# Optimization experiments

Measured on AMD Instinct MI355X. Metric: run time of the kernel, lower is better.

The kernel has to match this reference:

```python
import jax, jax.numpy as jnp
import numpy as np

B, N, E = 32, 128, 8192        # graphs, nodes/graph, edges total
IN, ED, H = 64, 32, 128        # node feat, edge feat, hidden
K1, K2, K3 = 64, 32, 16        # ceil(0.5*N) cascade from TopKPooling(ratio=0.5)
EPS = 1e-5


def setup_inputs():
    key = jax.random.key(0)
    ks = jax.random.split(key, 20)
    def rn(i, shape, s=1.0):
        return jax.random.normal(ks[i], shape, dtype=jnp.float32) * s
    x = rn(0, (B * N, IN))
    edge_attr = rn(1, (E, ED))
    epg = E // B  # edges per graph (intra-graph only)
    src = jax.random.randint(ks[2], (B, epg), 0, N)
    dst = jax.random.randint(ks[3], (B, epg), 0, N)
    off = (jnp.arange(B) * N)[:, None]
    edge_index = jnp.stack([(src + off).reshape(-1), (dst + off).reshape(-1)]).astype(jnp.int32)
    batch = jnp.repeat(jnp.arange(B), N).astype(jnp.int32)
    p = {}
    p['nn1_w'] = rn(4, (ED, IN * H), 0.05); p['nn1_b'] = jnp.zeros((IN * H,), jnp.float32)
    p['root1'] = rn(5, (IN, H), 0.1);       p['bias1'] = jnp.zeros((H,), jnp.float32)
    p['nn2_w'] = rn(6, (ED, H * H), 0.05);  p['nn2_b'] = jnp.zeros((H * H,), jnp.float32)
    p['root2'] = rn(7, (H, H), 0.1);        p['bias2'] = jnp.zeros((H,), jnp.float32)
    p['nn3_w'] = rn(8, (ED, H * H), 0.05);  p['nn3_b'] = jnp.zeros((H * H,), jnp.float32)
    p['root3'] = rn(9, (H, H), 0.1);        p['bias3'] = jnp.zeros((H,), jnp.float32)
    for k in ('1', '2', '3'):
        p['gamma' + k] = jnp.ones((H,), jnp.float32)
        p['beta' + k] = jnp.zeros((H,), jnp.float32)
    p['pw1'] = rn(10, (H,), 0.1); p['pw2'] = rn(11, (H,), 0.1); p['pw3'] = rn(12, (H,), 0.1)
    p['lin1_w'] = rn(13, (H, H // 2), 0.1); p['lin1_b'] = jnp.zeros((H // 2,), jnp.float32)
    p['lin2_w'] = rn(14, (H // 2, 1), 0.1); p['lin2_b'] = jnp.zeros((1,), jnp.float32)
    return dict(x=x, edge_index=edge_index, edge_attr=edge_attr, batch=batch, **p)


def _nnconv(x, src, dst, emask, eattr, nn_w, nn_b, root, bias, cin, cout, n_nodes):
    # per-edge weight matrix from edge MLP: [E, cin, cout]
    w = (eattr @ nn_w + nn_b).reshape(-1, cin, cout)
    msg = jnp.einsum('ei,eio->eo', x[src], w) * emask[:, None]  # per-edge matvec
    agg = jnp.zeros((n_nodes, cout), x.dtype).at[dst].add(msg)  # scatter-add aggr
    return agg + x @ root + bias


def _bn(x, gamma, beta):
    mu = x.mean(0)
    var = x.var(0)
    return gamma * (x - mu) * jax.lax.rsqrt(var + EPS) + beta


def _topk_pool(x, src, dst, emask, pw, nb, npg, k):
    # PyG TopKPooling: score = tanh((x.p)/||p||); keep top ceil(ratio*n) per graph
    score = jnp.tanh((x @ pw) / jnp.linalg.norm(pw))            # [nb*npg]
    _, idx = jax.lax.top_k(score.reshape(nb, npg), k)           # [nb, k]
    perm = (idx + (jnp.arange(nb) * npg)[:, None]).reshape(-1)  # global node ids
    x_new = x[perm] * score[perm][:, None]
    mapping = jnp.full((nb * npg,), -1, jnp.int32).at[perm].set(
        jnp.arange(nb * k, dtype=jnp.int32))
    ns, nd = mapping[src], mapping[dst]
    valid = (ns >= 0) & (nd >= 0) & emask   # filter_adj via mask, static shapes
    return x_new, jnp.where(valid, ns, 0), jnp.where(valid, nd, 0), valid


def _forward(x, edge_attr, nn1_w, nn1_b, root1, bias1, gamma1, beta1, pw1,
             nn2_w, nn2_b, root2, bias2, gamma2, beta2, pw2,
             nn3_w, nn3_b, root3, bias3, gamma3, beta3, pw3,
             lin1_w, lin1_b, lin2_w, lin2_b, edge_index):
    src0, dst0 = edge_index[0], edge_index[1]
    m0 = jnp.ones((E,), bool)
    h = _nnconv(x, src0, dst0, m0, edge_attr, nn1_w, nn1_b, root1, bias1, IN, H, B * N)
    h = jax.nn.relu(_bn(h, gamma1, beta1))
    h, s1, d1, m1 = _topk_pool(h, src0, dst0, m0, pw1, B, N, K1)
    h = _nnconv(h, s1, d1, m1, edge_attr, nn2_w, nn2_b, root2, bias2, H, H, B * K1)
    h = jax.nn.relu(_bn(h, gamma2, beta2))
    h, s2, d2, m2 = _topk_pool(h, s1, d1, m1, pw2, B, K1, K2)
    h = _nnconv(h, s2, d2, m2, edge_attr, nn3_w, nn3_b, root3, bias3, H, H, B * K2)
    h = jax.nn.relu(_bn(h, gamma3, beta3))
    h, _, _, _ = _topk_pool(h, s2, d2, m2, pw3, B, K2, K3)
    g = h.reshape(B, K3, H).mean(axis=1)          # global_mean_pool (equal-size graphs)
    g = jax.nn.relu(g @ lin1_w + lin1_b)          # dropout is identity in eval mode
    return jax.nn.sigmoid(g @ lin2_w + lin2_b)    # [B, 1]


def reference(x, edge_index, edge_attr, batch,
              nn1_w, nn1_b, root1, bias1, nn2_w, nn2_b, root2, bias2,
              nn3_w, nn3_b, root3, bias3, gamma1, beta1, gamma2, beta2,
              gamma3, beta3, pw1, pw2, pw3, lin1_w, lin1_b, lin2_w, lin2_b):
    return _forward(x, edge_attr, nn1_w, nn1_b, root1, bias1, gamma1, beta1, pw1,
                    nn2_w, nn2_b, root2, bias2, gamma2, beta2, pw2,
                    nn3_w, nn3_b, root3, bias3, gamma3, beta3, pw3,
                    lin1_w, lin1_b, lin2_w, lin2_b, edge_index)
```

## Files before the change

kernel.cpp:

```cpp
#include <hip/hip_runtime.h>

#define E_TOT 8192
#define NB    32
#define H     128
#define EPG   256
#define NDT   34
#define YD    33
#define YCOLS (YD * H)

#define KH1   2176
#define TROW1 (2 * KH1)
#define KSPLIT1 12

typedef __attribute__((ext_vector_type(8))) short bf16x8;
typedef __attribute__((ext_vector_type(4))) float f32x4;

__device__ __forceinline__ unsigned short bf16_rne(float f) {
    unsigned int u = __float_as_uint(f);
    unsigned int r = (u + 0x7FFFu + ((u >> 16) & 1u)) >> 16;
    return (unsigned short)r;
}
__device__ __forceinline__ float bf16_to_f32(unsigned short h) {
    return __uint_as_float(((unsigned int)h) << 16);
}

__device__ __forceinline__ void gload_lds16(const void* g, void* l) {
    __builtin_amdgcn_global_load_lds(
        (const __attribute__((address_space(1))) unsigned int*)g,
        (__attribute__((address_space(3))) unsigned int*)l, 16, 0, 0);
}

__device__ __forceinline__ void sig_done(int* cnt) {
    __syncthreads();
    if (threadIdx.x == 0) { __threadfence(); atomicAdd(cnt, 1); }
}
__device__ __forceinline__ void wait_done(int* cnt, int target) {
    if (threadIdx.x == 0)
        while (atomicAdd(cnt, 0) < target) __builtin_amdgcn_s_sleep(8);
    __syncthreads();
    __threadfence();
}

union PrepSMem {
    struct { unsigned short HI[128][72]; unsigned short LO[128][72]; } b1;
    struct { unsigned short HI[128][40]; unsigned short LO[128][40]; } bt;
    struct { float xL[128][64]; float eaL[256][32]; short srcL[256];
             short lists[16][256]; int cnt[16]; } t1;
};

__global__ __launch_bounds__(256)
void prep_all(const float* __restrict__ x, const float* __restrict__ ea,
              const int* __restrict__ esrc, const int* __restrict__ edst,
              const float* __restrict__ nn1w, const float* __restrict__ nn1b,
              const float* __restrict__ root1,
              const float* __restrict__ nn2w, const float* __restrict__ nn2b,
              const float* __restrict__ root2,
              const float* __restrict__ nn3w, const float* __restrict__ nn3b,
              const float* __restrict__ root3,
              unsigned short* __restrict__ Bt1, unsigned short* __restrict__ Bt2,
              unsigned short* __restrict__ Bt3, unsigned short* __restrict__ T1,
              float* __restrict__ stats, int* __restrict__ cnts)
{
    __shared__ PrepSMem sm;
    const int b   = blockIdx.x;
    const int tid = threadIdx.x;

    if (b < 34) {
        if (b == 0) {
            for (int i = tid; i < 768; i += 256) stats[i] = 0.f;
            if (tid < 8) cnts[tid] = 0;
        }
        const int d = b;
        const float* __restrict__ W =
            (d < 32) ? (nn1w + (size_t)d * 8192) : ((d == 32) ? nn1b : root1);
        for (int idx = tid; idx < 64 * 128; idx += 256) {
            const int ii = idx >> 7, o = idx & 127;
            const float v = W[ii * 128 + o];
            const unsigned short h = bf16_rne(v);
            sm.b1.HI[o][ii] = h;
            sm.b1.LO[o][ii] = bf16_rne(v - bf16_to_f32(h));
        }
        __syncthreads();
        const int o = tid & 127, half = tid >> 7;
        const uint4* s4 = (const uint4*)(half ? &sm.b1.LO[o][0] : &sm.b1.HI[o][0]);
        uint4* d4 = (uint4*)(Bt1 + (size_t)o * TROW1 + (half ? KH1 : 0) + d * 64);
        #pragma unroll
        for (int q = 0; q < 8; ++q) d4[q] = s4[q];
    } else if (b < 306) {
        const int unit  = b - 34;
        const int stage = unit / 136;
        const int u2    = unit - stage * 136;
        const int d  = u2 >> 2;
        const int i0 = (u2 & 3) * 32;
        const float* __restrict__ W = (stage == 0)
            ? ((d < 32) ? (nn2w + (size_t)d * 16384) : ((d == 32) ? nn2b : root2))
            : ((d < 32) ? (nn3w + (size_t)d * 16384) : ((d == 32) ? nn3b : root3));
        unsigned short* __restrict__ Bt = (stage == 0) ? Bt2 : Bt3;

        for (int idx = tid; idx < 32 * 128; idx += 256) {
            const int ii = idx >> 7, o = idx & 127;
            const float v = W[(size_t)(i0 + ii) * 128 + o];
            const unsigned short h = bf16_rne(v);
            sm.bt.HI[o][ii] = h;
            sm.bt.LO[o][ii] = bf16_rne(v - bf16_to_f32(h));
        }
        __syncthreads();
        const int o = tid & 127, half = tid >> 7;
        unsigned short* dst = Bt + (size_t)(d * 128 + o) * 384;
        const uint4* hs = (const uint4*)&sm.bt.HI[o][0];
        const uint4* ls = (const uint4*)&sm.bt.LO[o][0];
        if (half == 0) {
            uint4* p = (uint4*)(dst + i0);
            p[0] = hs[0]; p[1] = hs[1]; p[2] = hs[2]; p[3] = hs[3];
            uint4* q = (uint4*)(dst + 256 + i0);
            q[0] = ls[0]; q[1] = ls[1]; q[2] = ls[2]; q[3] = ls[3];
        } else {
            uint4* p = (uint4*)(dst + 128 + i0);
            p[0] = hs[0]; p[1] = hs[1]; p[2] = hs[2]; p[3] = hs[3];
        }
    } else {
        const int u    = b - 306;
        const int g    = u >> 3;
        const int base = (u & 7) * 16;
        const int wv   = tid >> 6;
        const int ln   = tid & 63;

        if (tid < 16) sm.t1.cnt[tid] = 0;
        for (int idx = tid; idx < 128 * 64; idx += 256)
            sm.t1.xL[idx >> 6][idx & 63] = x[(size_t)g * 8192 + idx];
        for (int idx = tid; idx < 256 * 32; idx += 256)
            sm.t1.eaL[idx >> 5][idx & 31] = ea[(size_t)g * 8192 + idx];
        __syncthreads();

        {
            const int e = tid;
            sm.t1.srcL[e] = (short)(esrc[g * EPG + e] - g * 128);
            const int r = (edst[g * EPG + e] - g * 128) - base;
            if (r >= 0 && r < 16) {
                const int pos = atomicAdd(&sm.t1.cnt[r], 1);
                sm.t1.lists[r][pos] = (short)e;
            }
        }
        __syncthreads();

        #pragma unroll
        for (int j = 0; j < 4; ++j) {
            const int r = wv * 4 + j;
            const int uu = base + r;
            float acc[33];
            #pragma unroll
            for (int d = 0; d < 33; ++d) acc[d] = 0.f;

            const int n = sm.t1.cnt[r];
            for (int t = 0; t < n; ++t) {
                const int e = sm.t1.lists[r][t];
                const float xv = sm.t1.xL[sm.t1.srcL[e]][ln];
                #pragma unroll
                for (int d = 0; d < 32; ++d) acc[d] += sm.t1.eaL[e][d] * xv;
                acc[32] += xv;
            }

            unsigned short* row = T1 + (size_t)(g * 128 + uu) * TROW1;
            #pragma unroll
            for (int d = 0; d < 33; ++d) {
                const unsigned short hb = bf16_rne(acc[d]);
                row[d * 64 + ln] = hb;
                row[KH1 + d * 64 + ln] = bf16_rne(acc[d] - bf16_to_f32(hb));
            }
            const float xv = sm.t1.xL[uu][ln];
            const unsigned short hb = bf16_rne(xv);
            row[2112 + ln] = hb;
            row[KH1 + 2112 + ln] = bf16_rne(xv - bf16_to_f32(hb));
        }
    }
}

__global__ __launch_bounds__(256)
void hgemm1(const unsigned short* __restrict__ A,
            const unsigned short* __restrict__ Bt,
            const float* __restrict__ bias,
            float* __restrict__ hpart)
{
    __shared__ unsigned short Alds[128 * 32];
    __shared__ unsigned short Blds[128 * 32];

    const int lane = threadIdx.x & 63;
    const int w    = threadIdx.x >> 6;
    const int wm = w >> 1, wn = w & 1;
    const int v0 = blockIdx.x * 128;
    const int c  = blockIdx.y;

    f32x4 acc[4][4];
    #pragma unroll
    for (int i = 0; i < 4; ++i)
        #pragma unroll
        for (int j = 0; j < 4; ++j)
            acc[i][j] = (f32x4)(0.0f);

    const int arow = lane >> 2;
    const int acol = (lane & 3) * 8;
    const int koff = (lane >> 4) * 8;
    const int mrow = lane & 15;

    for (int t = c * 17; t < c * 17 + 17; ++t) {
        const int s  = t / 68;
        const int ko = (t - s * 68) * 32;
        const int aoff = (s == 2 ? KH1 : 0) + ko;
        const int boff = (s == 1 ? KH1 : 0) + ko;

        __syncthreads();
        #pragma unroll
        for (int tt = 0; tt < 2; ++tt) {
            const int cc = w * 2 + tt;
            const int r = cc * 16 + arow;
            gload_lds16(A  + (size_t)(v0 + r) * TROW1 + aoff + acol, &Alds[cc * 512]);
            gload_lds16(Bt + (size_t)r * TROW1 + boff + acol, &Blds[cc * 512]);
        }
        __syncthreads();

        bf16x8 a[4], b[4];
        #pragma unroll
        for (int f = 0; f < 4; ++f) {
            a[f] = *(const bf16x8*)&Alds[(wm * 64 + f * 16 + mrow) * 32 + koff];
            b[f] = *(const bf16x8*)&Blds[(wn * 64 + f * 16 + mrow) * 32 + koff];
        }
        #pragma unroll
        for (int fm = 0; fm < 4; ++fm)
            #pragma unroll
            for (int fn = 0; fn < 4; ++fn)
                acc[fm][fn] = __builtin_amdgcn_mfma_f32_16x16x32_bf16(
                    a[fm], b[fn], acc[fm][fn], 0, 0, 0);
    }

    float* out = hpart + (size_t)c * (4096 * 128);
    const int crow = (lane >> 4) * 4;
    const int ccol = lane & 15;
    #pragma unroll
    for (int fm = 0; fm < 4; ++fm) {
        const int gr = v0 + wm * 64 + fm * 16 + crow;
        #pragma unroll
        for (int fn = 0; fn < 4; ++fn) {
            const int col = wn * 64 + fn * 16 + ccol;
            const float bv = (c == 0) ? bias[col] : 0.f;
            #pragma unroll
            for (int r = 0; r < 4; ++r)
                out[(size_t)(gr + r) * H + col] = acc[fm][fn][r] + bv;
        }
    }
}

__global__ __launch_bounds__(256)
void hsum(const float* __restrict__ hpart, float* __restrict__ h1)
{
    const int idx = blockIdx.x * 256 + threadIdx.x;
    const float4* src = (const float4*)hpart;
    float4 v = src[idx];
    #pragma unroll
    for (int c = 1; c < KSPLIT1; ++c) {
        const float4 p = src[(size_t)c * (4096 * 32) + idx];
        v.x += p.x; v.y += p.y; v.z += p.z; v.w += p.w;
    }
    ((float4*)h1)[idx] = v;
}

template<int K3>
__global__ __launch_bounds__(256)
void ygemm_mfma(const unsigned short* __restrict__ A,
                const unsigned short* __restrict__ Bt,
                float* __restrict__ Y,
                const float* __restrict__ bias,
                float* __restrict__ h)
{
    __shared__ unsigned short Alds[128 * 32];
    __shared__ unsigned short Blds[128 * 32];

    const int lane = threadIdx.x & 63;
    const int w    = threadIdx.x >> 6;
    const int wm = w >> 1, wn = w & 1;
    const int v0 = blockIdx.x * 128;
    const int n0 = blockIdx.y * 128;

    f32x4 acc[4][4];
    #pragma unroll
    for (int i = 0; i < 4; ++i)
        #pragma unroll
        for (int j = 0; j < 4; ++j)
            acc[i][j] = (f32x4)(0.0f);

    const int arow = lane >> 2;
    const int acol = (lane & 3) * 8;
    const int koff = (lane >> 4) * 8;
    const int mrow = lane & 15;

    for (int k0 = 0; k0 < K3; k0 += 32) {
        __syncthreads();
        #pragma unroll
        for (int t = 0; t < 2; ++t) {
            const int c = w * 2 + t;
            const int r = c * 16 + arow;
            gload_lds16(A  + (size_t)(v0 + r) * K3 + k0 + acol, &Alds[c * 512]);
            gload_lds16(Bt + (size_t)(n0 + r) * K3 + k0 + acol, &Blds[c * 512]);
        }
        __syncthreads();

        bf16x8 a[4], b[4];
        #pragma unroll
        for (int f = 0; f < 4; ++f) {
            a[f] = *(const bf16x8*)&Alds[(wm * 64 + f * 16 + mrow) * 32 + koff];
            b[f] = *(const bf16x8*)&Blds[(wn * 64 + f * 16 + mrow) * 32 + koff];
        }
        #pragma unroll
        for (int fm = 0; fm < 4; ++fm)
            #pragma unroll
            for (int fn = 0; fn < 4; ++fn)
                acc[fm][fn] = __builtin_amdgcn_mfma_f32_16x16x32_bf16(
                    a[fm], b[fn], acc[fm][fn], 0, 0, 0);
    }

    const int crow = (lane >> 4) * 4;
    const int ccol = lane & 15;
    const bool is_root = (blockIdx.y == YD);
    #pragma unroll
    for (int fm = 0; fm < 4; ++fm) {
        const int gr = v0 + wm * 64 + fm * 16 + crow;
        #pragma unroll
        for (int fn = 0; fn < 4; ++fn) {
            const int col = wn * 64 + fn * 16 + ccol;
            if (is_root) {
                const float bv = bias[col];
                #pragma unroll
                for (int r = 0; r < 4; ++r)
                    h[(size_t)(gr + r) * H + col] = acc[fm][fn][r] + bv;
            } else {
                const size_t gc = (size_t)blockIdx.y * H + col;
                #pragma unroll
                for (int r = 0; r < 4; ++r)
                    Y[(size_t)(gr + r) * YCOLS + gc] = acc[fm][fn][r];
            }
        }
    }
}

__global__ __launch_bounds__(256)
void contract_edges(const float* __restrict__ Y,
                    const float* __restrict__ ea,
                    const int*   __restrict__ esrc,
                    const int*   __restrict__ edst,
                    float*       __restrict__ agg)
{
    const int grp = threadIdx.x >> 5;
    const int l5  = threadIdx.x & 31;
    const int e   = blockIdx.x * 8 + grp;
    const int s   = esrc[e];
    if (s < 0) return;

    const float* yb  = Y + (size_t)s * YCOLS + l5 * 4;
    const float* ear = ea + (size_t)e * 32;

    float4 acc = *reinterpret_cast<const float4*>(yb + 32 * H);
    #pragma unroll 8
    for (int dd = 0; dd < 32; ++dd) {
        const float c = ear[dd];
        const float4 y = *reinterpret_cast<const float4*>(yb + dd * H);
        acc.x += c * y.x; acc.y += c * y.y; acc.z += c * y.z; acc.w += c * y.w;
    }
    float* out = agg + (size_t)edst[e] * H + l5 * 4;
    atomicAdd(out + 0, acc.x);
    atomicAdd(out + 1, acc.y);
    atomicAdd(out + 2, acc.z);
    atomicAdd(out + 3, acc.w);
}

__device__ void bn_stats_body(int nb, int bid, const float* __restrict__ h, int n,
                              float* __restrict__ gsum, float* __restrict__ gsumsq)
{
    __shared__ float sh[256];
    const int tid   = threadIdx.x;
    const int col   = tid & 127;
    const int rhalf = tid >> 7;
    float s = 0.f, sq = 0.f;
    for (int r = bid * 2 + rhalf; r < n; r += nb * 2) {
        float v = h[(size_t)r * H + col];
        s += v; sq += v * v;
    }
    sh[tid] = s;  __syncthreads();
    if (rhalf == 0) s += sh[tid + 128];
    __syncthreads();
    sh[tid] = sq; __syncthreads();
    if (rhalf == 0) {
        sq += sh[tid + 128];
        atomicAdd(&gsum[col], s);
        atomicAdd(&gsumsq[col], sq);
    }
    __syncthreads();
}

__device__ void pool_body(int g, const float* __restrict__ h,
                          const float* __restrict__ gsum, const float* __restrict__ gsumsq,
                          float n_f,
                          const float* __restrict__ gamma, const float* __restrict__ beta,
                          const float* __restrict__ pw,
                          int npg, int k,
                          const int* __restrict__ esrc_in, const int* __restrict__ edst_in,
                          int* __restrict__ esrc_out, int* __restrict__ edst_out,
                          unsigned short* __restrict__ Aout)
{
    const int tid = threadIdx.x;
    const int wv  = tid >> 6;
    const int ln  = tid & 63;

    __shared__ float muL[128], rsL[128], gmL[128], btL[128], pwL[128];
    __shared__ float scoreL[128], red[128];
    __shared__ int   mapL[128];
    __shared__ float sinv;

    if (tid < 128) {
        const float mu  = gsum[tid] / n_f;
        const float var = gsumsq[tid] / n_f - mu * mu;
        muL[tid] = mu;
        rsL[tid] = rsqrtf(var + 1e-5f);
        gmL[tid] = gamma[tid];
        btL[tid] = beta[tid];
        const float p = pw[tid];
        pwL[tid] = p;
        red[tid] = p * p;
    }
    __syncthreads();
    for (int off = 64; off > 0; off >>= 1) {
        if (tid < off) red[tid] += red[tid + off];
        __syncthreads();
    }
    if (tid == 0) sinv = rsqrtf(red[0]);
    __syncthreads();

    for (int r = wv; r < npg; r += 4) {
        const float* hr = h + (size_t)(g * npg + r) * H;
        float p = 0.f;
        #pragma unroll
        for (int half = 0; half < 2; ++half) {
            const int c = ln + half * 64;
            const float y = fmaxf(gmL[c] * (hr[c] - muL[c]) * rsL[c] + btL[c], 0.f);
            p += y * pwL[c];
        }
        #pragma unroll
        for (int off = 32; off > 0; off >>= 1)
            p += __shfl_down(p, off, 64);
        if (ln == 0) scoreL[r] = tanhf(p * sinv);
    }
    __syncthreads();

    if (tid < npg) {
        const float si = scoreL[tid];
        int cnt = 0;
        for (int j = 0; j < npg; ++j) {
            const float sj = scoreL[j];
            cnt += (sj > si) || (sj == si && j < tid);
        }
        mapL[tid] = (cnt < k) ? cnt : -1;
    }
    __syncthreads();

    for (int r = wv; r < npg; r += 4) {
        const int nr = mapL[r];
        if (nr < 0) continue;
        const float sc = scoreL[r];
        const float* hr = h + (size_t)(g * npg + r) * H;
        unsigned short* arow = Aout + (size_t)(g * k + nr) * 384;
        #pragma unroll
        for (int half = 0; half < 2; ++half) {
            const int c = ln + half * 64;
            const float y = fmaxf(gmL[c] * (hr[c] - muL[c]) * rsL[c] + btL[c], 0.f) * sc;
            const unsigned short hb = bf16_rne(y);
            const unsigned short lb = bf16_rne(y - bf16_to_f32(hb));
            arow[c] = hb; arow[128 + c] = hb; arow[256 + c] = lb;
        }
    }

    {
        const int e = g * EPG + tid;
        const int s = esrc_in[e];
        int ns = -1, nd = -1;
        if (s >= 0) {
            const int ms = mapL[s - g * npg];
            const int md = mapL[edst_in[e] - g * npg];
            if (ms >= 0 && md >= 0) { ns = g * k + ms; nd = g * k + md; }
        }
        esrc_out[e] = ns; edst_out[e] = nd;
    }
}

__device__ void pool_final_body(int g, const float* __restrict__ h,
                                const float* __restrict__ gsum, const float* __restrict__ gsumsq,
                                float n_f,
                                const float* __restrict__ gamma, const float* __restrict__ beta,
                                const float* __restrict__ pw,
                                const float* __restrict__ lin1_w, const float* __restrict__ lin1_b,
                                const float* __restrict__ lin2_w, const float* __restrict__ lin2_b,
                                float* __restrict__ out)
{
    const int tid = threadIdx.x;
    const int wv  = tid >> 6;
    const int ln  = tid & 63;
    const int npg = 32, k = 16;

    __shared__ float muL[128], rsL[128], gmL[128], btL[128], pwL[128];
    __shared__ float scoreL[32], red[128], gmean[128], h1c[64];
    __shared__ int   mapL[32];
    __shared__ float sinv;

    if (tid < 128) {
        const float mu  = gsum[tid] / n_f;
        const float var = gsumsq[tid] / n_f - mu * mu;
        muL[tid] = mu;
        rsL[tid] = rsqrtf(var + 1e-5f);
        gmL[tid] = gamma[tid];
        btL[tid] = beta[tid];
        const float p = pw[tid];
        pwL[tid] = p;
        red[tid] = p * p;
    }
    __syncthreads();
    for (int off = 64; off > 0; off >>= 1) {
        if (tid < off) red[tid] += red[tid + off];
        __syncthreads();
    }
    if (tid == 0) sinv = rsqrtf(red[0]);
    __syncthreads();

    for (int r = wv; r < npg; r += 4) {
        const float* hr = h + (size_t)(g * npg + r) * H;
        float p = 0.f;
        #pragma unroll
        for (int half = 0; half < 2; ++half) {
            const int c = ln + half * 64;
            const float y = fmaxf(gmL[c] * (hr[c] - muL[c]) * rsL[c] + btL[c], 0.f);
            p += y * pwL[c];
        }
        #pragma unroll
        for (int off = 32; off > 0; off >>= 1)
            p += __shfl_down(p, off, 64);
        if (ln == 0) scoreL[r] = tanhf(p * sinv);
    }
    __syncthreads();

    if (tid < npg) {
        const float si = scoreL[tid];
        int cnt = 0;
        for (int j = 0; j < npg; ++j) {
            const float sj = scoreL[j];
            cnt += (sj > si) || (sj == si && j < tid);
        }
        mapL[tid] = (cnt < k) ? cnt : -1;
    }
    __syncthreads();

    if (tid < 128) {
        float acc = 0.f;
        for (int r = 0; r < npg; ++r) {
            if (mapL[r] < 0) continue;
            const float hv = h[(size_t)(g * npg + r) * H + tid];
            const float y  = fmaxf(gmL[tid] * (hv - muL[tid]) * rsL[tid] + btL[tid], 0.f);
            acc += y * scoreL[r];
        }
        gmean[tid] = acc * (1.0f / 16.0f);
    }
    __syncthreads();

    if (tid < 64) {
        float acc = lin1_b[tid];
        for (int o = 0; o < 128; ++o) acc += gmean[o] * lin1_w[o * 64 + tid];
        h1c[tid] = fmaxf(acc, 0.f);
    }
    __syncthreads();
    if (tid == 0) {
        float z = lin2_b[0];
        for (int j = 0; j < 64; ++j) z += h1c[j] * lin2_w[j];
        out[g] = 1.0f / (1.0f + expf(-z));
    }
}

__global__ __launch_bounds__(256)
void mega_bp(const float* __restrict__ h, int n, float n_f,
             float* __restrict__ stats,
             const float* __restrict__ gamma, const float* __restrict__ beta,
             const float* __restrict__ pw, int npg, int k,
             const int* __restrict__ esrc_in, const int* __restrict__ edst_in,
             int* __restrict__ esrc_out, int* __restrict__ edst_out,
             unsigned short* __restrict__ Aout, int* __restrict__ cnt)
{
    bn_stats_body(256, blockIdx.x, h, n, stats, stats + 128);
    sig_done(cnt);
    if (blockIdx.x < NB) {
        wait_done(cnt, 256);
        pool_body(blockIdx.x, h, stats, stats + 128, n_f, gamma, beta, pw,
                  npg, k, esrc_in, edst_in, esrc_out, edst_out, Aout);
    }
}

__global__ __launch_bounds__(256)
void mega_bp_final(const float* __restrict__ h,
                   float* __restrict__ stats,
                   const float* __restrict__ gamma, const float* __restrict__ beta,
                   const float* __restrict__ pw,
                   const float* __restrict__ lin1_w, const float* __restrict__ lin1_b,
                   const float* __restrict__ lin2_w, const float* __restrict__ lin2_b,
                   float* __restrict__ out, int* __restrict__ cnt)
{
    bn_stats_body(256, blockIdx.x, h, 1024, stats, stats + 128);
    sig_done(cnt);
    if (blockIdx.x < NB) {
        wait_done(cnt, 256);
        pool_final_body(blockIdx.x, h, stats, stats + 128, 1024.0f, gamma, beta, pw,
                        lin1_w, lin1_b, lin2_w, lin2_b, out);
    }
}

extern "C" void kernel_launch(void* const* d_in, const int* in_sizes, int n_in,
                              void* d_out, int out_size, void* d_ws, size_t ws_size,
                              hipStream_t stream)
{
    const float* x        = (const float*)d_in[0];
    const int*   ei       = (const int*)  d_in[1];
    const float* eattr    = (const float*)d_in[2];
    const float* nn1_w    = (const float*)d_in[4];
    const float* nn1_b    = (const float*)d_in[5];
    const float* root1    = (const float*)d_in[6];
    const float* bias1    = (const float*)d_in[7];
    const float* nn2_w    = (const float*)d_in[8];
    const float* nn2_b    = (const float*)d_in[9];
    const float* root2    = (const float*)d_in[10];
    const float* bias2    = (const float*)d_in[11];
    const float* nn3_w    = (const float*)d_in[12];
    const float* nn3_b    = (const float*)d_in[13];
    const float* root3    = (const float*)d_in[14];
    const float* bias3    = (const float*)d_in[15];
    const float* gamma1   = (const float*)d_in[16];
    const float* beta1    = (const float*)d_in[17];
    const float* gamma2   = (const float*)d_in[18];
    const float* beta2    = (const float*)d_in[19];
    const float* gamma3   = (const float*)d_in[20];
    const float* beta3    = (const float*)d_in[21];
    const float* pw1      = (const float*)d_in[22];
    const float* pw2      = (const float*)d_in[23];
    const float* pw3      = (const float*)d_in[24];
    const float* lin1_w   = (const float*)d_in[25];
    const float* lin1_b   = (const float*)d_in[26];
    const float* lin2_w   = (const float*)d_in[27];
    const float* lin2_b   = (const float*)d_in[28];

    const int* ei_src = ei;
    const int* ei_dst = ei + E_TOT;

    char* wp = (char*)d_ws;
    auto alloc = [&](size_t bytes) { char* p = wp; wp += (bytes + 255) & ~(size_t)255; return p; };
    float* h1   = (float*)alloc(4096 * 128 * 4);
    float* h2   = (float*)alloc(2048 * 128 * 4);
    float* h3   = (float*)alloc(1024 * 128 * 4);
    int*   src1 = (int*)alloc(E_TOT * 4);
    int*   dst1 = (int*)alloc(E_TOT * 4);
    int*   src2 = (int*)alloc(E_TOT * 4);
    int*   dst2 = (int*)alloc(E_TOT * 4);
    float* stats = (float*)alloc(6 * 128 * 4);
    int*   cnts  = (int*)alloc(8 * 4);
    unsigned short* A2   = (unsigned short*)alloc((size_t)2048 * 384 * 2);
    unsigned short* A3   = (unsigned short*)alloc((size_t)1024 * 384 * 2);
    unsigned short* Bt1n = (unsigned short*)alloc((size_t)128 * TROW1 * 2);
    unsigned short* Bt2  = (unsigned short*)alloc((size_t)4352 * 384 * 2);
    unsigned short* Bt3  = (unsigned short*)alloc((size_t)4352 * 384 * 2);
    unsigned short* T1   = (unsigned short*)alloc((size_t)4096 * TROW1 * 2);
    float* hpart = (float*)alloc((size_t)KSPLIT1 * 4096 * 128 * 4);
    float* Ybuf  = (float*)alloc((size_t)2048 * YCOLS * 4);

    prep_all<<<562, 256, 0, stream>>>(x, eattr, ei_src, ei_dst,
                                      nn1_w, nn1_b, root1,
                                      nn2_w, nn2_b, root2,
                                      nn3_w, nn3_b, root3,
                                      Bt1n, Bt2, Bt3, T1, stats, cnts);

    hgemm1<<<dim3(32, KSPLIT1), 256, 0, stream>>>(T1, Bt1n, bias1, hpart);
    hsum<<<512, 256, 0, stream>>>(hpart, h1);
    mega_bp<<<256, 256, 0, stream>>>(h1, 4096, 4096.0f, stats,
                                     gamma1, beta1, pw1, 128, 64,
                                     ei_src, ei_dst, src1, dst1, A2, cnts);

    ygemm_mfma<384><<<dim3(16, NDT), 256, 0, stream>>>(A2, Bt2, Ybuf, bias2, h2);
    contract_edges<<<E_TOT / 8, 256, 0, stream>>>(Ybuf, eattr, src1, dst1, h2);
    mega_bp<<<256, 256, 0, stream>>>(h2, 2048, 2048.0f, stats + 256,
                                     gamma2, beta2, pw2, 64, 32,
                                     src1, dst1, src2, dst2, A3, cnts + 1);

    ygemm_mfma<384><<<dim3(8, NDT), 256, 0, stream>>>(A3, Bt3, Ybuf, bias3, h3);
    contract_edges<<<E_TOT / 8, 256, 0, stream>>>(Ybuf, eattr, src2, dst2, h3);
    mega_bp_final<<<256, 256, 0, stream>>>(h3, stats + 512,
                                           gamma3, beta3, pw3,
                                           lin1_w, lin1_b, lin2_w, lin2_b,
                                           (float*)d_out, cnts + 2);
}
```

Before: 305.3 us.

## Split top-k pooling across all blocks with a second grid barrier

```diff
diff --git a/kernel.cpp b/kernel.cpp
--- a/kernel.cpp
+++ b/kernel.cpp
@@ -395,23 +395,20 @@
     __syncthreads();
 }
 
-__device__ void pool_body(int g, const float* __restrict__ h,
-                          const float* __restrict__ gsum, const float* __restrict__ gsumsq,
-                          float n_f,
-                          const float* __restrict__ gamma, const float* __restrict__ beta,
-                          const float* __restrict__ pw,
-                          int npg, int k,
-                          const int* __restrict__ esrc_in, const int* __restrict__ edst_in,
-                          int* __restrict__ esrc_out, int* __restrict__ edst_out,
-                          unsigned short* __restrict__ Aout)
-{
+__device__ void score_body(int bid, const float* __restrict__ h,
+                           const float* __restrict__ gsum, const float* __restrict__ gsumsq,
+                           float n_f,
+                           const float* __restrict__ gamma, const float* __restrict__ beta,
+                           const float* __restrict__ pw,
+                           int npg, float* __restrict__ scoreG)
+{
+    const int g   = bid >> 3;
+    const int sub = bid & 7;
     const int tid = threadIdx.x;
     const int wv  = tid >> 6;
     const int ln  = tid & 63;
 
-    __shared__ float muL[128], rsL[128], gmL[128], btL[128], pwL[128];
-    __shared__ float scoreL[128], red[128];
-    __shared__ int   mapL[128];
+    __shared__ float muL[128], rsL[128], gmL[128], btL[128], pwL[128], red[128];
     __shared__ float sinv;
 
     if (tid < 128) {
@@ -433,7 +430,8 @@
     if (tid == 0) sinv = rsqrtf(red[0]);
     __syncthreads();
 
-    for (int r = wv; r < npg; r += 4) {
+    const int rps = npg >> 3;
+    for (int r = sub * rps + wv; r < (sub + 1) * rps; r += 4) {
         const float* hr = h + (size_t)(g * npg + r) * H;
         float p = 0.f;
         #pragma unroll
@@ -445,68 +443,29 @@
         #pragma unroll
         for (int off = 32; off > 0; off >>= 1)
             p += __shfl_down(p, off, 64);
-        if (ln == 0) scoreL[r] = tanhf(p * sinv);
-    }
-    __syncthreads();
-
-    if (tid < npg) {
-        const float si = scoreL[tid];
-        int cnt = 0;
-        for (int j = 0; j < npg; ++j) {
-            const float sj = scoreL[j];
-            cnt += (sj > si) || (sj == si && j < tid);
-        }
-        mapL[tid] = (cnt < k) ? cnt : -1;
-    }
-    __syncthreads();
-
-    for (int r = wv; r < npg; r += 4) {
-        const int nr = mapL[r];
-        if (nr < 0) continue;
-        const float sc = scoreL[r];
-        const float* hr = h + (size_t)(g * npg + r) * H;
-        unsigned short* arow = Aout + (size_t)(g * k + nr) * 384;
-        #pragma unroll
-        for (int half = 0; half < 2; ++half) {
-            const int c = ln + half * 64;
-            const float y = fmaxf(gmL[c] * (hr[c] - muL[c]) * rsL[c] + btL[c], 0.f) * sc;
-            const unsigned short hb = bf16_rne(y);
-            const unsigned short lb = bf16_rne(y - bf16_to_f32(hb));
-            arow[c] = hb; arow[128 + c] = hb; arow[256 + c] = lb;
-        }
-    }
-
-    {
-        const int e = g * EPG + tid;
-        const int s = esrc_in[e];
-        int ns = -1, nd = -1;
-        if (s >= 0) {
-            const int ms = mapL[s - g * npg];
-            const int md = mapL[edst_in[e] - g * npg];
-            if (ms >= 0 && md >= 0) { ns = g * k + ms; nd = g * k + md; }
-        }
-        esrc_out[e] = ns; edst_out[e] = nd;
-    }
-}
-
-__device__ void pool_final_body(int g, const float* __restrict__ h,
-                                const float* __restrict__ gsum, const float* __restrict__ gsumsq,
-                                float n_f,
-                                const float* __restrict__ gamma, const float* __restrict__ beta,
-                                const float* __restrict__ pw,
-                                const float* __restrict__ lin1_w, const float* __restrict__ lin1_b,
-                                const float* __restrict__ lin2_w, const float* __restrict__ lin2_b,
-                                float* __restrict__ out)
-{
+        if (ln == 0) scoreG[g * 128 + r] = tanhf(p * sinv);
+    }
+}
+
+__device__ void emit_body(int bid, const float* __restrict__ h,
+                          const float* __restrict__ gsum, const float* __restrict__ gsumsq,
+                          float n_f,
+                          const float* __restrict__ gamma, const float* __restrict__ beta,
+                          int npg, int k,
+                          const float* __restrict__ scoreG,
+                          const int* __restrict__ esrc_in, const int* __restrict__ edst_in,
+                          int* __restrict__ esrc_out, int* __restrict__ edst_out,
+                          unsigned short* __restrict__ Aout)
+{
+    const int g   = bid >> 3;
+    const int sub = bid & 7;
     const int tid = threadIdx.x;
     const int wv  = tid >> 6;
     const int ln  = tid & 63;
-    const int npg = 32, k = 16;
-
-    __shared__ float muL[128], rsL[128], gmL[128], btL[128], pwL[128];
-    __shared__ float scoreL[32], red[128], gmean[128], h1c[64];
-    __shared__ int   mapL[32];
-    __shared__ float sinv;
+
+    __shared__ float muL[128], rsL[128], gmL[128], btL[128];
+    __shared__ float scoreL[128];
+    __shared__ int   mapL[128];
 
     if (tid < 128) {
         const float mu  = gsum[tid] / n_f;
@@ -515,32 +474,76 @@
         rsL[tid] = rsqrtf(var + 1e-5f);
         gmL[tid] = gamma[tid];
         btL[tid] = beta[tid];
-        const float p = pw[tid];
-        pwL[tid] = p;
-        red[tid] = p * p;
-    }
-    __syncthreads();
-    for (int off = 64; off > 0; off >>= 1) {
-        if (tid < off) red[tid] += red[tid + off];
-        __syncthreads();
-    }
-    if (tid == 0) sinv = rsqrtf(red[0]);
-    __syncthreads();
-
-    for (int r = wv; r < npg; r += 4) {
+        if (tid < npg) scoreL[tid] = scoreG[g * 128 + tid];
+    }
+    __syncthreads();
+
+    if (tid < npg) {
+        const float si = scoreL[tid];
+        int cnt = 0;
+        for (int j = 0; j < npg; ++j) {
+            const float sj = scoreL[j];
+            cnt += (sj > si) || (sj == si && j < tid);
+        }
+        mapL[tid] = (cnt < k) ? cnt : -1;
+    }
+    __syncthreads();
+
+    const int rps = npg >> 3;
+    for (int r = sub * rps + wv; r < (sub + 1) * rps; r += 4) {
+        const int nr = mapL[r];
+        if (nr < 0) continue;
+        const float sc = scoreL[r];
         const float* hr = h + (size_t)(g * npg + r) * H;
-        float p = 0.f;
+        unsigned short* arow = Aout + (size_t)(g * k + nr) * 384;
         #pragma unroll
         for (int half = 0; half < 2; ++half) {
             const int c = ln + half * 64;
-            const float y = fmaxf(gmL[c] * (hr[c] - muL[c]) * rsL[c] + btL[c], 0.f);
-            p += y * pwL[c];
-        }
-        #pragma unroll
-        for (int off = 32; off > 0; off >>= 1)
-            p += __shfl_down(p, off, 64);
-        if (ln == 0) scoreL[r] = tanhf(p * sinv);
-    }
+            const float y = fmaxf(gmL[c] * (hr[c] - muL[c]) * rsL[c] + btL[c], 0.f) * sc;
+            const unsigned short hb = bf16_rne(y);
+            const unsigned short lb = bf16_rne(y - bf16_to_f32(hb));
+            arow[c] = hb; arow[128 + c] = hb; arow[256 + c] = lb;
+        }
+    }
+
+    if (tid < 32) {
+        const int e = g * EPG + sub * 32 + tid;
+        const int s = esrc_in[e];
+        int ns = -1, nd = -1;
+        if (s >= 0) {
+            const int ms = mapL[s - g * npg];
+            const int md = mapL[edst_in[e] - g * npg];
+            if (ms >= 0 && md >= 0) { ns = g * k + ms; nd = g * k + md; }
+        }
+        esrc_out[e] = ns; edst_out[e] = nd;
+    }
+}
+
+__device__ void final_tail_body(int g, const float* __restrict__ h,
+                                const float* __restrict__ gsum, const float* __restrict__ gsumsq,
+                                float n_f,
+                                const float* __restrict__ gamma, const float* __restrict__ beta,
+                                const float* __restrict__ scoreG,
+                                const float* __restrict__ lin1_w, const float* __restrict__ lin1_b,
+                                const float* __restrict__ lin2_w, const float* __restrict__ lin2_b,
+                                float* __restrict__ out)
+{
+    const int tid = threadIdx.x;
+    const int npg = 32, k = 16;
+
+    __shared__ float muL[128], rsL[128], gmL[128], btL[128];
+    __shared__ float scoreL[32], gmean[128], h1c[64];
+    __shared__ int   mapL[32];
+
+    if (tid < 128) {
+        const float mu  = gsum[tid] / n_f;
+        const float var = gsumsq[tid] / n_f - mu * mu;
+        muL[tid] = mu;
+        rsL[tid] = rsqrtf(var + 1e-5f);
+        gmL[tid] = gamma[tid];
+        btL[tid] = beta[tid];
+    }
+    if (tid < 32) scoreL[tid] = scoreG[g * 128 + tid];
     __syncthreads();
 
     if (tid < npg) {
@@ -586,15 +589,17 @@
              const float* __restrict__ pw, int npg, int k,
              const int* __restrict__ esrc_in, const int* __restrict__ edst_in,
              int* __restrict__ esrc_out, int* __restrict__ edst_out,
-             unsigned short* __restrict__ Aout, int* __restrict__ cnt)
+             unsigned short* __restrict__ Aout, float* __restrict__ scoreG,
+             int* __restrict__ cnt)
 {
     bn_stats_body(256, blockIdx.x, h, n, stats, stats + 128);
     sig_done(cnt);
-    if (blockIdx.x < NB) {
-        wait_done(cnt, 256);
-        pool_body(blockIdx.x, h, stats, stats + 128, n_f, gamma, beta, pw,
-                  npg, k, esrc_in, edst_in, esrc_out, edst_out, Aout);
-    }
+    wait_done(cnt, 256);
+    score_body(blockIdx.x, h, stats, stats + 128, n_f, gamma, beta, pw, npg, scoreG);
+    sig_done(cnt + 1);
+    wait_done(cnt + 1, 256);
+    emit_body(blockIdx.x, h, stats, stats + 128, n_f, gamma, beta, npg, k,
+              scoreG, esrc_in, edst_in, esrc_out, edst_out, Aout);
 }
 
 __global__ __launch_bounds__(256)
@@ -604,14 +609,18 @@
                    const float* __restrict__ pw,
                    const float* __restrict__ lin1_w, const float* __restrict__ lin1_b,
                    const float* __restrict__ lin2_w, const float* __restrict__ lin2_b,
-                   float* __restrict__ out, int* __restrict__ cnt)
+                   float* __restrict__ out, float* __restrict__ scoreG,
+                   int* __restrict__ cnt)
 {
     bn_stats_body(256, blockIdx.x, h, 1024, stats, stats + 128);
     sig_done(cnt);
+    wait_done(cnt, 256);
+    score_body(blockIdx.x, h, stats, stats + 128, 1024.0f, gamma, beta, pw, 32, scoreG);
+    sig_done(cnt + 1);
     if (blockIdx.x < NB) {
-        wait_done(cnt, 256);
-        pool_final_body(blockIdx.x, h, stats, stats + 128, 1024.0f, gamma, beta, pw,
-                        lin1_w, lin1_b, lin2_w, lin2_b, out);
+        wait_done(cnt + 1, 256);
+        final_tail_body(blockIdx.x, h, stats, stats + 128, 1024.0f, gamma, beta,
+                        scoreG, lin1_w, lin1_b, lin2_w, lin2_b, out);
     }
 }
 
@@ -662,6 +671,7 @@
     int*   dst2 = (int*)alloc(E_TOT * 4);
     float* stats = (float*)alloc(6 * 128 * 4);
     int*   cnts  = (int*)alloc(8 * 4);
+    float* scoreG = (float*)alloc(NB * 128 * 4);
     unsigned short* A2   = (unsigned short*)alloc((size_t)2048 * 384 * 2);
     unsigned short* A3   = (unsigned short*)alloc((size_t)1024 * 384 * 2);
     unsigned short* Bt1n = (unsigned short*)alloc((size_t)128 * TROW1 * 2);
@@ -681,18 +691,18 @@
     hsum<<<512, 256, 0, stream>>>(hpart, h1);
     mega_bp<<<256, 256, 0, stream>>>(h1, 4096, 4096.0f, stats,
                                      gamma1, beta1, pw1, 128, 64,
-                                     ei_src, ei_dst, src1, dst1, A2, cnts);
+                                     ei_src, ei_dst, src1, dst1, A2, scoreG, cnts);
 
     ygemm_mfma<384><<<dim3(16, NDT), 256, 0, stream>>>(A2, Bt2, Ybuf, bias2, h2);
     contract_edges<<<E_TOT / 8, 256, 0, stream>>>(Ybuf, eattr, src1, dst1, h2);
     mega_bp<<<256, 256, 0, stream>>>(h2, 2048, 2048.0f, stats + 256,
                                      gamma2, beta2, pw2, 64, 32,
-                                     src1, dst1, src2, dst2, A3, cnts + 1);
+                                     src1, dst1, src2, dst2, A3, scoreG, cnts + 2);
 
     ygemm_mfma<384><<<dim3(8, NDT), 256, 0, stream>>>(A3, Bt3, Ybuf, bias3, h3);
     contract_edges<<<E_TOT / 8, 256, 0, stream>>>(Ybuf, eattr, src2, dst2, h3);
     mega_bp_final<<<256, 256, 0, stream>>>(h3, stats + 512,
                                            gamma3, beta3, pw3,
                                            lin1_w, lin1_b, lin2_w, lin2_b,
-                                           (float*)d_out, cnts + 2);
-}
+                                           (float*)d_out, scoreG, cnts + 4);
+}
```

New measurement: 396.8 us. 1.3x slower.
